# Kernel optimization log

Hardware: AMD Instinct MI355X
Metric: run time of the kernel (lower is better)

## Reference

```python
import jax, jax.numpy as jnp
import numpy as np

N = 50000    # num_nodes
E = 800000   # num_edges
IN = 256     # input_dim
H = 256      # hidden_dim
EPS = 1e-5   # BatchNorm eps


def setup_inputs() -> dict:
    key = jax.random.key(0)
    ks = jax.random.split(key, 12)
    def nrm(k, shp, s=0.05):
        return jax.random.normal(k, shp, dtype=jnp.float32) * s
    return {
        "x": jax.random.normal(ks[0], (N, IN), dtype=jnp.float32),
        "edge_index": jax.random.randint(ks[1], (2, E), 0, N, dtype=jnp.int32),
        "edge_weight": jax.random.uniform(ks[2], (E,), dtype=jnp.float32),
        # GCNConv 1 / 2 (PyG stores weight as [in, out]; bias [out])
        "W1": nrm(ks[3], (IN, H)), "b1": jnp.zeros((H,), jnp.float32),
        "W2": nrm(ks[4], (H, H)), "b2": jnp.zeros((H,), jnp.float32),
        # BatchNorm1d 1 / 2
        "gamma1": jnp.ones((H,), jnp.float32), "beta1": jnp.zeros((H,), jnp.float32),
        "gamma2": jnp.ones((H,), jnp.float32), "beta2": jnp.zeros((H,), jnp.float32),
        # LSTM 1 (input 2H) and LSTM 2 (input H), PyTorch gate order i,f,g,o
        "Wih1": nrm(ks[5], (4 * H, 2 * H)), "Whh1": nrm(ks[6], (4 * H, H)),
        "bih1": jnp.zeros((4 * H,), jnp.float32), "bhh1": jnp.zeros((4 * H,), jnp.float32),
        "Wih2": nrm(ks[7], (4 * H, H)), "Whh2": nrm(ks[8], (4 * H, H)),
        "bih2": jnp.zeros((4 * H,), jnp.float32), "bhh2": jnp.zeros((4 * H,), jnp.float32),
    }


def reference(x, edge_index, edge_weight, W1, b1, W2, b2, gamma1, beta1,
              gamma2, beta2, Wih1, Whh1, bih1, bhh1, Wih2, Whh2, bih2, bhh2):
    src, dst = edge_index[0], edge_index[1]
    # GCN symmetric normalization with added self-loops (fill value 1.0)
    loops = jnp.arange(N, dtype=src.dtype)
    src_a = jnp.concatenate([src, loops])
    dst_a = jnp.concatenate([dst, loops])
    ew_a = jnp.concatenate([edge_weight, jnp.ones((N,), edge_weight.dtype)])
    deg = jax.ops.segment_sum(ew_a, dst_a, num_segments=N)
    deg_safe = jnp.where(deg > 0, deg, 1.0)
    dinv = jnp.where(deg > 0, jax.lax.rsqrt(deg_safe), 0.0)
    norm = dinv[src_a] * ew_a * dinv[dst_a]  # [E+N]

    def gcn(h, W, b):
        m = (h @ W)[src_a] * norm[:, None]               # gather + scale messages
        return jax.ops.segment_sum(m, dst_a, num_segments=N) + b

    def bn(h, g, bta):  # training-mode BatchNorm1d (batch stats, biased var)
        mu = jnp.mean(h, axis=0)
        var = jnp.mean((h - mu) ** 2, axis=0)
        return (h - mu) * jax.lax.rsqrt(var + EPS) * g + bta

    def lstm_step0(inp, Wih, bih, bhh):  # single step from h0=c0=0 (window=1)
        gates = inp @ Wih.T + bih + bhh  # Whh term vanishes since h0=0
        i, f, g, o = jnp.split(gates, 4, axis=-1)
        c = jax.nn.sigmoid(i) * jnp.tanh(g)  # f*c0 = 0
        return jax.nn.sigmoid(o) * jnp.tanh(c)

    h1 = bn(jax.nn.relu(gcn(x, W1, b1)), gamma1, beta1)   # [N, H]
    h2 = bn(jax.nn.relu(gcn(h1, W2, b2)), gamma2, beta2)  # [N, H]
    Xc = jnp.concatenate([h1, h2], axis=1)                # [N, 2H]
    hL1 = lstm_step0(Xc, Wih1, bih1, bhh1)                # LSTM1 final hidden
    hL2 = lstm_step0(hL1, Wih2, bih2, bhh2)               # LSTM2 final hidden
    # S with window=1 reduces to x itself
    return jnp.concatenate([hL1, hL2, x], axis=1)         # [N, 2H + IN]
```

## Files before the change

kernel.cpp:

```cpp
#include <hip/hip_runtime.h>
#include <math.h>

#define NN 50000
#define NE 800000
#define LDP 40

typedef __attribute__((ext_vector_type(8))) short bf8;
typedef __attribute__((ext_vector_type(4))) float f32x4;

__device__ __forceinline__ float sigm(float x){ return 1.f/(1.f+expf(-x)); }
__device__ __forceinline__ unsigned short f2b(float f){
  union{float f;unsigned u;} v; v.f=f;
  unsigned r=v.u+0x7fff+((v.u>>16)&1u);
  return (unsigned short)(r>>16);
}
__device__ __forceinline__ float b2f(unsigned short h){
  union{unsigned u;float f;} v; v.u=((unsigned)h)<<16; return v.f;
}

__global__ __launch_bounds__(256) void k_init(float* deg,int* cnt,float* colsum,float* colsq){
  int i=blockIdx.x*256+threadIdx.x;
  if(i<NN){deg[i]=1.0f;cnt[i]=0;}
  if(i<256){colsum[i]=0.f;colsq[i]=0.f;}
}

__global__ __launch_bounds__(256) void k_deg(const int* __restrict__ ei,const float* __restrict__ ew,
                                             float* deg,int* cnt){
  int e=blockIdx.x*256+threadIdx.x;
  if(e<NE){int d=ei[NE+e];atomicAdd(&deg[d],ew[e]);atomicAdd(&cnt[d],1);}
}

__global__ __launch_bounds__(256) void k_dinv(const float* __restrict__ deg,float* dinv){
  int i=blockIdx.x*256+threadIdx.x;
  if(i<NN){float d=deg[i];dinv[i]=d>0.f?rsqrtf(d):0.f;}
}

__global__ __launch_bounds__(1024) void k_scan(const int* __restrict__ cnt,int* row_ptr,int* cursor){
  __shared__ int s[1024];
  __shared__ int carry;
  int tid=threadIdx.x;
  if(tid==0)carry=0;
  __syncthreads();
  for(int base=0;base<NN;base+=1024){
    int i=base+tid;
    int v=(i<NN)?cnt[i]:0;
    s[tid]=v;__syncthreads();
    for(int off=1;off<1024;off<<=1){
      int t=(tid>=off)?s[tid-off]:0;
      __syncthreads();
      s[tid]+=t;__syncthreads();
    }
    int excl=carry+s[tid]-v;
    if(i<NN){row_ptr[i]=excl;cursor[i]=excl;}
    __syncthreads();
    if(tid==1023)carry+=s[1023];
    __syncthreads();
  }
  if(tid==0)row_ptr[NN]=carry;
}

__global__ __launch_bounds__(256) void k_scatter(const int* __restrict__ ei,const float* __restrict__ ew,
    const float* __restrict__ dinv,int* cursor,int* csr_src,float* csr_w){
  int e=blockIdx.x*256+threadIdx.x;
  if(e<NE){
    int s=ei[e],d=ei[NE+e];
    float wv=dinv[s]*ew[e]*dinv[d];
    int p=atomicAdd(&cursor[d],1);
    csr_src[p]=s;csr_w[p]=wv;
  }
}

__global__ __launch_bounds__(256) void k_wt(const float* __restrict__ W,unsigned short* __restrict__ Wt){
  int j=blockIdx.x,k=threadIdx.x;
  Wt[j*256+k]=f2b(W[k*256+j]);
}
__global__ __launch_bounds__(256) void k_f2b(const float* __restrict__ s,unsigned short* __restrict__ d,int n){
  int i=blockIdx.x*256+threadIdx.x;
  if(i<n)d[i]=f2b(s[i]);
}
__global__ __launch_bounds__(256) void k_bsum(const float* __restrict__ a,const float* __restrict__ b,
                                              float* __restrict__ s,int n){
  int i=blockIdx.x*256+threadIdx.x;
  if(i<n)s[i]=a[i]+b[i];
}

template<typename TA>
__global__ __launch_bounds__(256,2) void k_gemm_mfma(
    const TA* __restrict__ A,int lda,const unsigned short* __restrict__ Bt,int K,
    unsigned short* __restrict__ Cb){
  __shared__ unsigned short As[128*LDP];
  __shared__ unsigned short Bs[128*LDP];
  int tid=threadIdx.x;
  int row0=blockIdx.x*128,col0=blockIdx.y*128;
  int lane=tid&63,l15=lane&15,quad=lane>>4;
  int wid=tid>>6,wm=wid>>1,wn=wid&1;
  f32x4 acc[4][4]={};
  for(int k0=0;k0<K;k0+=32){
    if constexpr(sizeof(TA)==4){
      int r=tid>>3,ks=(tid&7)*4;
      #pragma unroll
      for(int rr=0;rr<4;rr++){
        int row=row0+rr*32+r;
        float4 v=make_float4(0.f,0.f,0.f,0.f);
        if(row<NN)v=*(const float4*)&A[(long)row*lda+k0+ks];
        ushort4 h;h.x=f2b(v.x);h.y=f2b(v.y);h.z=f2b(v.z);h.w=f2b(v.w);
        *(ushort4*)&As[(rr*32+r)*LDP+ks]=h;
      }
    }else{
      int r=tid>>2,ks=(tid&3)*8;
      #pragma unroll
      for(int rr=0;rr<2;rr++){
        int row=row0+rr*64+r;
        bf8 v=(bf8)(short)0;
        if(row<NN)v=*(const bf8*)&A[(long)row*lda+k0+ks];
        *(bf8*)&As[(rr*64+r)*LDP+ks]=v;
      }
    }
    { int r=tid>>2,ks=(tid&3)*8;
      #pragma unroll
      for(int rr=0;rr<2;rr++){
        bf8 v=*(const bf8*)&Bt[(long)(col0+rr*64+r)*K+k0+ks];
        *(bf8*)&Bs[(rr*64+r)*LDP+ks]=v;
      }
    }
    __syncthreads();
    bf8 af[4],bfg[4];
    #pragma unroll
    for(int i=0;i<4;i++){
      af[i]=*(const bf8*)&As[(wm*64+i*16+l15)*LDP+quad*8];
      bfg[i]=*(const bf8*)&Bs[(wn*64+i*16+l15)*LDP+quad*8];
    }
    #pragma unroll
    for(int mi=0;mi<4;mi++)
      #pragma unroll
      for(int ni=0;ni<4;ni++)
        acc[mi][ni]=__builtin_amdgcn_mfma_f32_16x16x32_bf16(af[mi],bfg[ni],acc[mi][ni],0,0,0);
    __syncthreads();
  }
  #pragma unroll
  for(int mi=0;mi<4;mi++){
    #pragma unroll
    for(int r=0;r<4;r++){
      int node=row0+wm*64+mi*16+quad*4+r;
      if(node>=NN)continue;
      #pragma unroll
      for(int ni=0;ni<4;ni++){
        int col=col0+wn*64+ni*16+l15;
        Cb[(long)node*256+col]=f2b(acc[mi][ni][r]);
      }
    }
  }
}

__global__ __launch_bounds__(256,2) void k_lstm_mfma(
    const unsigned short* __restrict__ A,int lda,int K,
    const unsigned short* __restrict__ Wb,const float* __restrict__ bsum,
    float* __restrict__ Hout,int ldh,unsigned short* __restrict__ Hb){
  __shared__ unsigned short As[128*LDP];
  __shared__ unsigned short Bs[3*64*LDP];
  int tid=threadIdx.x;
  int row0=blockIdx.x*128,m0=blockIdx.y*64;
  int lane=tid&63,l15=lane&15,quad=lane>>4;
  int wid=tid>>6,wm=wid>>1,wn=wid&1;
  f32x4 ai[4][2]={},ag[4][2]={},ao[4][2]={};
  for(int k0=0;k0<K;k0+=32){
    { int r=tid>>2,ks=(tid&3)*8;
      #pragma unroll
      for(int rr=0;rr<2;rr++){
        int row=row0+rr*64+r;
        bf8 v=(bf8)(short)0;
        if(row<NN)v=*(const bf8*)&A[(long)row*lda+k0+ks];
        *(bf8*)&As[(rr*64+r)*LDP+ks]=v;
      }
      bf8 v0=*(const bf8*)&Wb[(long)(  0+m0+r)*K+k0+ks];
      bf8 v1=*(const bf8*)&Wb[(long)(512+m0+r)*K+k0+ks];
      bf8 v2=*(const bf8*)&Wb[(long)(768+m0+r)*K+k0+ks];
      *(bf8*)&Bs[(0*64+r)*LDP+ks]=v0;
      *(bf8*)&Bs[(1*64+r)*LDP+ks]=v1;
      *(bf8*)&Bs[(2*64+r)*LDP+ks]=v2;
    }
    __syncthreads();
    bf8 af[4],bi[2],bg[2],bo[2];
    #pragma unroll
    for(int i=0;i<4;i++)af[i]=*(const bf8*)&As[(wm*64+i*16+l15)*LDP+quad*8];
    #pragma unroll
    for(int ni=0;ni<2;ni++){
      int rr=wn*32+ni*16+l15;
      bi[ni]=*(const bf8*)&Bs[(0*64+rr)*LDP+quad*8];
      bg[ni]=*(const bf8*)&Bs[(1*64+rr)*LDP+quad*8];
      bo[ni]=*(const bf8*)&Bs[(2*64+rr)*LDP+quad*8];
    }
    #pragma unroll
    for(int mi=0;mi<4;mi++)
      #pragma unroll
      for(int ni=0;ni<2;ni++){
        ai[mi][ni]=__builtin_amdgcn_mfma_f32_16x16x32_bf16(af[mi],bi[ni],ai[mi][ni],0,0,0);
        ag[mi][ni]=__builtin_amdgcn_mfma_f32_16x16x32_bf16(af[mi],bg[ni],ag[mi][ni],0,0,0);
        ao[mi][ni]=__builtin_amdgcn_mfma_f32_16x16x32_bf16(af[mi],bo[ni],ao[mi][ni],0,0,0);
      }
    __syncthreads();
  }
  #pragma unroll
  for(int ni=0;ni<2;ni++){
    int m=m0+wn*32+ni*16+l15;
    float b_i=bsum[m],b_g=bsum[512+m],b_o=bsum[768+m];
    #pragma unroll
    for(int mi=0;mi<4;mi++){
      #pragma unroll
      for(int r=0;r<4;r++){
        int node=row0+wm*64+mi*16+quad*4+r;
        if(node>=NN)continue;
        float gi=ai[mi][ni][r]+b_i;
        float gg=ag[mi][ni][r]+b_g;
        float go=ao[mi][ni][r]+b_o;
        float c=sigm(gi)*tanhf(gg);
        float h=sigm(go)*tanhf(c);
        Hout[(long)node*ldh+m]=h;
        if(Hb)Hb[(long)node*256+m]=f2b(h);
      }
    }
  }
}

__global__ __launch_bounds__(256) void k_spmm(const unsigned short* __restrict__ Tb,
    const int* __restrict__ row_ptr,const int* __restrict__ csr_src,const float* __restrict__ csr_w,
    const float* __restrict__ dinv,const float* __restrict__ bias,
    unsigned short* __restrict__ Xb,float* colsum,float* colsq){
  __shared__ float s_sum[4][256];
  __shared__ float s_sq[4][256];
  int tid=threadIdx.x;
  int lane=tid&63,wv=tid>>6;
  int c4=lane*4;
  float4 bc=*(const float4*)&bias[c4];
  float sum0=0.f,sum1=0.f,sum2=0.f,sum3=0.f;
  float sq0=0.f,sq1=0.f,sq2=0.f,sq3=0.f;
  int rowbase=blockIdx.x*32+wv*8;
  #pragma unroll 1
  for(int pr=0;pr<4;pr++){
    int ra=rowbase+pr*2,rb=ra+1;
    bool va=ra<NN,vb=rb<NN;
    int raa=va?ra:0,rbb=vb?rb:0;
    int p0a=row_ptr[raa],p1a=row_ptr[raa+1];
    int p0b=row_ptr[rbb],p1b=row_ptr[rbb+1];
    int la=va?(p1a-p0a):0,lb=vb?(p1b-p0b):0;
    float dia=dinv[raa],dib=dinv[rbb];
    ushort4 tsa=*(const ushort4*)&Tb[(long)raa*256+c4];
    ushort4 tsb=*(const ushort4*)&Tb[(long)rbb*256+c4];
    float wsa=dia*dia,wsb=dib*dib;
    float a0=wsa*b2f(tsa.x),a1=wsa*b2f(tsa.y),a2=wsa*b2f(tsa.z),a3=wsa*b2f(tsa.w);
    float b0=wsb*b2f(tsb.x),b1=wsb*b2f(tsb.y),b2=wsb*b2f(tsb.z),b3=wsb*b2f(tsb.w);
    int L=max(la,lb);
    for(int j=0;j<L;j++){
      int ia=j<la?(p0a+j):p0a;
      int ib=j<lb?(p0b+j):p0b;
      float wa=j<la?csr_w[ia]:0.f;
      float wb=j<lb?csr_w[ib]:0.f;
      int sa=csr_src[ia];sa=min(max(sa,0),NN-1);
      int sb=csr_src[ib];sb=min(max(sb,0),NN-1);
      ushort4 ta=*(const ushort4*)&Tb[(long)sa*256+c4];
      ushort4 tb=*(const ushort4*)&Tb[(long)sb*256+c4];
      a0+=wa*b2f(ta.x);a1+=wa*b2f(ta.y);a2+=wa*b2f(ta.z);a3+=wa*b2f(ta.w);
      b0+=wb*b2f(tb.x);b1+=wb*b2f(tb.y);b2+=wb*b2f(tb.z);b3+=wb*b2f(tb.w);
    }
    if(va){
      a0=fmaxf(a0+bc.x,0.f);a1=fmaxf(a1+bc.y,0.f);a2=fmaxf(a2+bc.z,0.f);a3=fmaxf(a3+bc.w,0.f);
      ushort4 o;o.x=f2b(a0);o.y=f2b(a1);o.z=f2b(a2);o.w=f2b(a3);
      *(ushort4*)&Xb[(long)ra*512+c4]=o;
      sum0+=a0;sum1+=a1;sum2+=a2;sum3+=a3;
      sq0+=a0*a0;sq1+=a1*a1;sq2+=a2*a2;sq3+=a3*a3;
    }
    if(vb){
      b0=fmaxf(b0+bc.x,0.f);b1=fmaxf(b1+bc.y,0.f);b2=fmaxf(b2+bc.z,0.f);b3=fmaxf(b3+bc.w,0.f);
      ushort4 o;o.x=f2b(b0);o.y=f2b(b1);o.z=f2b(b2);o.w=f2b(b3);
      *(ushort4*)&Xb[(long)rb*512+c4]=o;
      sum0+=b0;sum1+=b1;sum2+=b2;sum3+=b3;
      sq0+=b0*b0;sq1+=b1*b1;sq2+=b2*b2;sq3+=b3*b3;
    }
  }
  s_sum[wv][c4+0]=sum0;s_sum[wv][c4+1]=sum1;s_sum[wv][c4+2]=sum2;s_sum[wv][c4+3]=sum3;
  s_sq[wv][c4+0]=sq0;s_sq[wv][c4+1]=sq1;s_sq[wv][c4+2]=sq2;s_sq[wv][c4+3]=sq3;
  __syncthreads();
  if(tid<256){
    float a=s_sum[0][tid]+s_sum[1][tid]+s_sum[2][tid]+s_sum[3][tid];
    float q=s_sq[0][tid]+s_sq[1][tid]+s_sq[2][tid]+s_sq[3][tid];
    atomicAdd(&colsum[tid],a);
    atomicAdd(&colsq[tid],q);
  }
}

__global__ __launch_bounds__(256) void k_bnfin(const float* __restrict__ gamma,const float* __restrict__ beta,
    float* colsum,float* colsq,float* scale,float* shift){
  int c=threadIdx.x;
  float mu=colsum[c]/(float)NN;
  float var=colsq[c]/(float)NN-mu*mu;
  float r=rsqrtf(var+1e-5f);
  float sc=r*gamma[c];
  scale[c]=sc;
  shift[c]=beta[c]-mu*sc;
  colsum[c]=0.f;colsq[c]=0.f;
}

__global__ __launch_bounds__(256) void k_bnapply(unsigned short* __restrict__ Xb,
    const float* __restrict__ scale,const float* __restrict__ shift){
  long idx=(long)blockIdx.x*256+threadIdx.x;
  long r=idx>>6;int c=(int)(idx&63)*4;
  if(r<NN){
    ushort4 v=*(const ushort4*)&Xb[r*512+c];
    ushort4 w;
    w.x=f2b(b2f(v.x)*scale[c+0]+shift[c+0]);
    w.y=f2b(b2f(v.y)*scale[c+1]+shift[c+1]);
    w.z=f2b(b2f(v.z)*scale[c+2]+shift[c+2]);
    w.w=f2b(b2f(v.w)*scale[c+3]+shift[c+3]);
    *(ushort4*)&Xb[r*512+c]=w;
  }
}

__global__ __launch_bounds__(256) void k_copy_out(const float* __restrict__ src,
    float* __restrict__ out,int colofs){
  long idx=(long)blockIdx.x*256+threadIdx.x;
  long r=idx>>6;int cc=(int)(idx&63)*4;
  if(r<NN)*(float4*)&out[r*768+colofs+cc]=*(const float4*)&src[r*256+cc];
}

extern "C" void kernel_launch(void* const* d_in,const int* in_sizes,int n_in,
                              void* d_out,int out_size,void* d_ws,size_t ws_size,
                              hipStream_t stream){
  const float* x   =(const float*)d_in[0];
  const int*   ei  =(const int*)  d_in[1];
  const float* ew  =(const float*)d_in[2];
  const float* W1  =(const float*)d_in[3];
  const float* b1  =(const float*)d_in[4];
  const float* W2  =(const float*)d_in[5];
  const float* b2  =(const float*)d_in[6];
  const float* g1  =(const float*)d_in[7];
  const float* be1 =(const float*)d_in[8];
  const float* g2  =(const float*)d_in[9];
  const float* be2 =(const float*)d_in[10];
  const float* Wih1=(const float*)d_in[11];
  const float* bih1=(const float*)d_in[13];
  const float* bhh1=(const float*)d_in[14];
  const float* Wih2=(const float*)d_in[15];
  const float* bih2=(const float*)d_in[17];
  const float* bhh2=(const float*)d_in[18];
  float* out=(float*)d_out;

  char* w=(char*)d_ws;
  auto alloc=[&](size_t bytes)->char*{char* p=w;w+=(bytes+255)&~(size_t)255;return p;};
  float* deg    =(float*)alloc((size_t)NN*4);
  float* dinv   =(float*)alloc((size_t)NN*4);
  int*   cnt    =(int*)  alloc((size_t)NN*4);
  int*   row_ptr=(int*)  alloc((size_t)(NN+1)*4);
  int*   cursor =(int*)  alloc((size_t)NN*4);
  int*   csr_src=(int*)  alloc((size_t)NE*4);
  float* csr_w  =(float*)alloc((size_t)NE*4);
  float* colsum =(float*)alloc(256*4);
  float* colsq  =(float*)alloc(256*4);
  float* scale  =(float*)alloc(256*4);
  float* shift  =(float*)alloc(256*4);
  unsigned short* Xcb =(unsigned short*)alloc((size_t)NN*512*2);
  unsigned short* TbH =(unsigned short*)alloc((size_t)NN*256*2);
  unsigned short* Wt1 =(unsigned short*)alloc(256*256*2);
  unsigned short* Wt2 =(unsigned short*)alloc(256*256*2);
  unsigned short* Wb1 =(unsigned short*)alloc((size_t)1024*512*2);
  unsigned short* Wb2 =(unsigned short*)alloc((size_t)1024*256*2);
  float* bs1 =(float*)alloc(1024*4);
  float* bs2 =(float*)alloc(1024*4);

  int nb=(NN+255)/256;
  k_init<<<nb,256,0,stream>>>(deg,cnt,colsum,colsq);
  k_deg<<<(NE+255)/256,256,0,stream>>>(ei,ew,deg,cnt);
  k_dinv<<<nb,256,0,stream>>>(deg,dinv);
  k_scan<<<1,1024,0,stream>>>(cnt,row_ptr,cursor);
  k_scatter<<<(NE+255)/256,256,0,stream>>>(ei,ew,dinv,cursor,csr_src,csr_w);

  k_wt<<<256,256,0,stream>>>(W1,Wt1);
  k_wt<<<256,256,0,stream>>>(W2,Wt2);
  k_f2b<<<(1024*512+255)/256,256,0,stream>>>(Wih1,Wb1,1024*512);
  k_f2b<<<(1024*256+255)/256,256,0,stream>>>(Wih2,Wb2,1024*256);
  k_bsum<<<4,256,0,stream>>>(bih1,bhh1,bs1,1024);
  k_bsum<<<4,256,0,stream>>>(bih2,bhh2,bs2,1024);

  int ngx=(NN+127)/128;
  dim3 gd(ngx,2);
  dim3 gl(ngx,4);
  int nspmm=(NN+31)/32;

  k_gemm_mfma<float><<<gd,256,0,stream>>>(x,256,Wt1,256,TbH);
  k_spmm<<<nspmm,256,0,stream>>>(TbH,row_ptr,csr_src,csr_w,dinv,b1,Xcb+0,colsum,colsq);
  k_bnfin<<<1,256,0,stream>>>(g1,be1,colsum,colsq,scale,shift);
  k_bnapply<<<12500,256,0,stream>>>(Xcb+0,scale,shift);
  k_gemm_mfma<unsigned short><<<gd,256,0,stream>>>(Xcb,512,Wt2,256,TbH);
  k_spmm<<<nspmm,256,0,stream>>>(TbH,row_ptr,csr_src,csr_w,dinv,b2,Xcb+256,colsum,colsq);
  k_bnfin<<<1,256,0,stream>>>(g2,be2,colsum,colsq,scale,shift);
  k_bnapply<<<12500,256,0,stream>>>(Xcb+256,scale,shift);
  k_lstm_mfma<<<gl,256,0,stream>>>(Xcb,512,512,Wb1,bs1,out+0,768,TbH);
  k_lstm_mfma<<<gl,256,0,stream>>>(TbH,256,256,Wb2,bs2,out+256,768,nullptr);
  k_copy_out<<<12500,256,0,stream>>>(x,out,512);
}
```

Measured before the change: 909.2 us.

## Double-buffer GEMM/LSTM tiles via direct global-to-LDS loads with XOR swizzle

Rewrites the GEMM and LSTM MFMA kernels to stage A/B tiles with global_load_lds directly into a double-buffered, XOR-swizzled shared-memory layout. The next K-slice is prefetched while the current one is consumed, so there is a single barrier per iteration instead of a load-sync-compute-sync pattern. The fp32 input x is cast to bf16 once in a separate kernel so both GEMMs share one bf16 path, and the LSTM activations switch to fast exp/rcp approximations. This costs an extra cast pass and extra workspace, and row clamping replaces zero padding for out-of-range rows. The barrier ordering with asynchronous LDS loads may be fragile.

```diff
diff --git a/kernel.cpp b/kernel.cpp
--- a/kernel.cpp
+++ b/kernel.cpp
@@ -3,12 +3,11 @@
 
 #define NN 50000
 #define NE 800000
-#define LDP 40
 
 typedef __attribute__((ext_vector_type(8))) short bf8;
 typedef __attribute__((ext_vector_type(4))) float f32x4;
-
-__device__ __forceinline__ float sigm(float x){ return 1.f/(1.f+expf(-x)); }
+typedef unsigned int u32;
+
 __device__ __forceinline__ unsigned short f2b(float f){
   union{float f;unsigned u;} v; v.f=f;
   unsigned r=v.u+0x7fff+((v.u>>16)&1u);
@@ -16,6 +15,14 @@
 }
 __device__ __forceinline__ float b2f(unsigned short h){
   union{unsigned u;float f;} v; v.u=((unsigned)h)<<16; return v.f;
+}
+__device__ __forceinline__ float fsigm(float x){ return __builtin_amdgcn_rcpf(1.f+__expf(-x)); }
+__device__ __forceinline__ float ftanh(float x){ return 1.f-2.f*__builtin_amdgcn_rcpf(__expf(2.f*x)+1.f); }
+
+__device__ __forceinline__ void gload16(const unsigned short* g, unsigned short* l){
+  __builtin_amdgcn_global_load_lds((const __attribute__((address_space(1))) u32*)g,
+                                   (__attribute__((address_space(3))) u32*)l,
+                                   16,0,0);
 }
 
 __global__ __launch_bounds__(256) void k_init(float* deg,int* cnt,float* colsum,float* colsq){
@@ -78,57 +85,54 @@
   int i=blockIdx.x*256+threadIdx.x;
   if(i<n)d[i]=f2b(s[i]);
 }
+__global__ __launch_bounds__(256) void k_cast(const float* __restrict__ s,unsigned short* __restrict__ d){
+  long i=(long)blockIdx.x*256+threadIdx.x;
+  float4 v=*(const float4*)&s[i*4];
+  ushort4 o;o.x=f2b(v.x);o.y=f2b(v.y);o.z=f2b(v.z);o.w=f2b(v.w);
+  *(ushort4*)&d[i*4]=o;
+}
 __global__ __launch_bounds__(256) void k_bsum(const float* __restrict__ a,const float* __restrict__ b,
                                               float* __restrict__ s,int n){
   int i=blockIdx.x*256+threadIdx.x;
   if(i<n)s[i]=a[i]+b[i];
 }
 
-template<typename TA>
 __global__ __launch_bounds__(256,2) void k_gemm_mfma(
-    const TA* __restrict__ A,int lda,const unsigned short* __restrict__ Bt,int K,
+    const unsigned short* __restrict__ A,int lda,const unsigned short* __restrict__ Bt,int K,
     unsigned short* __restrict__ Cb){
-  __shared__ unsigned short As[128*LDP];
-  __shared__ unsigned short Bs[128*LDP];
+  __shared__ unsigned short As[2][4096];
+  __shared__ unsigned short Bs[2][4096];
   int tid=threadIdx.x;
   int row0=blockIdx.x*128,col0=blockIdx.y*128;
   int lane=tid&63,l15=lane&15,quad=lane>>4;
   int wid=tid>>6,wm=wid>>1,wn=wid&1;
+  int sr=tid>>2;
+  int aoff=((tid&3)^((tid>>3)&3))*8;
+  int xq=quad^((l15>>1)&3);
+  long ar0=row0+sr;    if(ar0>=NN)ar0=NN-1;
+  long ar1=row0+64+sr; if(ar1>=NN)ar1=NN-1;
+  const unsigned short* a0p=A+ar0*lda+aoff;
+  const unsigned short* a1p=A+ar1*lda+aoff;
+  const unsigned short* b0p=Bt+(long)(col0+sr)*K+aoff;
+  const unsigned short* b1p=Bt+(long)(col0+64+sr)*K+aoff;
+  int lb=wid*512;
   f32x4 acc[4][4]={};
-  for(int k0=0;k0<K;k0+=32){
-    if constexpr(sizeof(TA)==4){
-      int r=tid>>3,ks=(tid&7)*4;
-      #pragma unroll
-      for(int rr=0;rr<4;rr++){
-        int row=row0+rr*32+r;
-        float4 v=make_float4(0.f,0.f,0.f,0.f);
-        if(row<NN)v=*(const float4*)&A[(long)row*lda+k0+ks];
-        ushort4 h;h.x=f2b(v.x);h.y=f2b(v.y);h.z=f2b(v.z);h.w=f2b(v.w);
-        *(ushort4*)&As[(rr*32+r)*LDP+ks]=h;
-      }
-    }else{
-      int r=tid>>2,ks=(tid&3)*8;
-      #pragma unroll
-      for(int rr=0;rr<2;rr++){
-        int row=row0+rr*64+r;
-        bf8 v=(bf8)(short)0;
-        if(row<NN)v=*(const bf8*)&A[(long)row*lda+k0+ks];
-        *(bf8*)&As[(rr*64+r)*LDP+ks]=v;
-      }
-    }
-    { int r=tid>>2,ks=(tid&3)*8;
-      #pragma unroll
-      for(int rr=0;rr<2;rr++){
-        bf8 v=*(const bf8*)&Bt[(long)(col0+rr*64+r)*K+k0+ks];
-        *(bf8*)&Bs[(rr*64+r)*LDP+ks]=v;
-      }
-    }
-    __syncthreads();
+  int nt=K/32;
+  gload16(a0p,&As[0][lb]); gload16(a1p,&As[0][2048+lb]);
+  gload16(b0p,&Bs[0][lb]); gload16(b1p,&Bs[0][2048+lb]);
+  __syncthreads();
+  for(int t=0;t<nt;t++){
+    int cur=t&1;
+    if(t+1<nt){
+      int k0=(t+1)*32;int nxt=cur^1;
+      gload16(a0p+k0,&As[nxt][lb]); gload16(a1p+k0,&As[nxt][2048+lb]);
+      gload16(b0p+k0,&Bs[nxt][lb]); gload16(b1p+k0,&Bs[nxt][2048+lb]);
+    }
     bf8 af[4],bfg[4];
     #pragma unroll
     for(int i=0;i<4;i++){
-      af[i]=*(const bf8*)&As[(wm*64+i*16+l15)*LDP+quad*8];
-      bfg[i]=*(const bf8*)&Bs[(wn*64+i*16+l15)*LDP+quad*8];
+      af[i] =*(const bf8*)&As[cur][(wm*64+i*16+l15)*32+xq*8];
+      bfg[i]=*(const bf8*)&Bs[cur][(wn*64+i*16+l15)*32+xq*8];
     }
     #pragma unroll
     for(int mi=0;mi<4;mi++)
@@ -156,39 +160,44 @@
     const unsigned short* __restrict__ A,int lda,int K,
     const unsigned short* __restrict__ Wb,const float* __restrict__ bsum,
     float* __restrict__ Hout,int ldh,unsigned short* __restrict__ Hb){
-  __shared__ unsigned short As[128*LDP];
-  __shared__ unsigned short Bs[3*64*LDP];
+  __shared__ unsigned short As[2][4096];
+  __shared__ unsigned short Bs[2][6144];
   int tid=threadIdx.x;
   int row0=blockIdx.x*128,m0=blockIdx.y*64;
   int lane=tid&63,l15=lane&15,quad=lane>>4;
   int wid=tid>>6,wm=wid>>1,wn=wid&1;
+  int sr=tid>>2;
+  int aoff=((tid&3)^((tid>>3)&3))*8;
+  int xq=quad^((l15>>1)&3);
+  long ar0=row0+sr;    if(ar0>=NN)ar0=NN-1;
+  long ar1=row0+64+sr; if(ar1>=NN)ar1=NN-1;
+  const unsigned short* a0p=A+ar0*lda+aoff;
+  const unsigned short* a1p=A+ar1*lda+aoff;
+  const unsigned short* wip=Wb+(long)(    m0+sr)*K+aoff;
+  const unsigned short* wgp=Wb+(long)(512+m0+sr)*K+aoff;
+  const unsigned short* wop=Wb+(long)(768+m0+sr)*K+aoff;
+  int lb=wid*512;
   f32x4 ai[4][2]={},ag[4][2]={},ao[4][2]={};
-  for(int k0=0;k0<K;k0+=32){
-    { int r=tid>>2,ks=(tid&3)*8;
-      #pragma unroll
-      for(int rr=0;rr<2;rr++){
-        int row=row0+rr*64+r;
-        bf8 v=(bf8)(short)0;
-        if(row<NN)v=*(const bf8*)&A[(long)row*lda+k0+ks];
-        *(bf8*)&As[(rr*64+r)*LDP+ks]=v;
-      }
-      bf8 v0=*(const bf8*)&Wb[(long)(  0+m0+r)*K+k0+ks];
-      bf8 v1=*(const bf8*)&Wb[(long)(512+m0+r)*K+k0+ks];
-      bf8 v2=*(const bf8*)&Wb[(long)(768+m0+r)*K+k0+ks];
-      *(bf8*)&Bs[(0*64+r)*LDP+ks]=v0;
-      *(bf8*)&Bs[(1*64+r)*LDP+ks]=v1;
-      *(bf8*)&Bs[(2*64+r)*LDP+ks]=v2;
-    }
-    __syncthreads();
+  int nt=K/32;
+  gload16(a0p,&As[0][lb]); gload16(a1p,&As[0][2048+lb]);
+  gload16(wip,&Bs[0][lb]); gload16(wgp,&Bs[0][2048+lb]); gload16(wop,&Bs[0][4096+lb]);
+  __syncthreads();
+  for(int t=0;t<nt;t++){
+    int cur=t&1;
+    if(t+1<nt){
+      int k0=(t+1)*32;int nxt=cur^1;
+      gload16(a0p+k0,&As[nxt][lb]); gload16(a1p+k0,&As[nxt][2048+lb]);
+      gload16(wip+k0,&Bs[nxt][lb]); gload16(wgp+k0,&Bs[nxt][2048+lb]); gload16(wop+k0,&Bs[nxt][4096+lb]);
+    }
     bf8 af[4],bi[2],bg[2],bo[2];
     #pragma unroll
-    for(int i=0;i<4;i++)af[i]=*(const bf8*)&As[(wm*64+i*16+l15)*LDP+quad*8];
+    for(int i=0;i<4;i++)af[i]=*(const bf8*)&As[cur][(wm*64+i*16+l15)*32+xq*8];
     #pragma unroll
     for(int ni=0;ni<2;ni++){
       int rr=wn*32+ni*16+l15;
-      bi[ni]=*(const bf8*)&Bs[(0*64+rr)*LDP+quad*8];
-      bg[ni]=*(const bf8*)&Bs[(1*64+rr)*LDP+quad*8];
-      bo[ni]=*(const bf8*)&Bs[(2*64+rr)*LDP+quad*8];
+      bi[ni]=*(const bf8*)&Bs[cur][(    rr)*32+xq*8];
+      bg[ni]=*(const bf8*)&Bs[cur][( 64+rr)*32+xq*8];
+      bo[ni]=*(const bf8*)&Bs[cur][(128+rr)*32+xq*8];
     }
     #pragma unroll
     for(int mi=0;mi<4;mi++)
@@ -213,8 +222,8 @@
         float gi=ai[mi][ni][r]+b_i;
         float gg=ag[mi][ni][r]+b_g;
         float go=ao[mi][ni][r]+b_o;
-        float c=sigm(gi)*tanhf(gg);
-        float h=sigm(go)*tanhf(c);
+        float c=fsigm(gi)*ftanh(gg);
+        float h=fsigm(go)*ftanh(c);
         Hout[(long)node*ldh+m]=h;
         if(Hb)Hb[(long)node*256+m]=f2b(h);
       }
@@ -359,6 +368,7 @@
   float* shift  =(float*)alloc(256*4);
   unsigned short* Xcb =(unsigned short*)alloc((size_t)NN*512*2);
   unsigned short* TbH =(unsigned short*)alloc((size_t)NN*256*2);
+  unsigned short* xb  =(unsigned short*)alloc((size_t)NN*256*2);
   unsigned short* Wt1 =(unsigned short*)alloc(256*256*2);
   unsigned short* Wt2 =(unsigned short*)alloc(256*256*2);
   unsigned short* Wb1 =(unsigned short*)alloc((size_t)1024*512*2);
@@ -375,6 +385,7 @@
 
   k_wt<<<256,256,0,stream>>>(W1,Wt1);
   k_wt<<<256,256,0,stream>>>(W2,Wt2);
+  k_cast<<<12500,256,0,stream>>>(x,xb);
   k_f2b<<<(1024*512+255)/256,256,0,stream>>>(Wih1,Wb1,1024*512);
   k_f2b<<<(1024*256+255)/256,256,0,stream>>>(Wih2,Wb2,1024*256);
   k_bsum<<<4,256,0,stream>>>(bih1,bhh1,bs1,1024);
@@ -385,11 +396,11 @@
   dim3 gl(ngx,4);
   int nspmm=(NN+31)/32;
 
-  k_gemm_mfma<float><<<gd,256,0,stream>>>(x,256,Wt1,256,TbH);
+  k_gemm_mfma<<<gd,256,0,stream>>>(xb,256,Wt1,256,TbH);
   k_spmm<<<nspmm,256,0,stream>>>(TbH,row_ptr,csr_src,csr_w,dinv,b1,Xcb+0,colsum,colsq);
   k_bnfin<<<1,256,0,stream>>>(g1,be1,colsum,colsq,scale,shift);
   k_bnapply<<<12500,256,0,stream>>>(Xcb+0,scale,shift);
-  k_gemm_mfma<unsigned short><<<gd,256,0,stream>>>(Xcb,512,Wt2,256,TbH);
+  k_gemm_mfma<<<gd,256,0,stream>>>(Xcb,512,Wt2,256,TbH);
   k_spmm<<<nspmm,256,0,stream>>>(TbH,row_ptr,csr_src,csr_w,dinv,b2,Xcb+256,colsum,colsq);
   k_bnfin<<<1,256,0,stream>>>(g2,be2,colsum,colsq,scale,shift);
   k_bnapply<<<12500,256,0,stream>>>(Xcb+256,scale,shift);
```

Result: faster. 863.3 us (-5.0%).
